# Performance work log

Hardware: AMD Instinct MI355X
Metric: run time of the kernel (lower is better)

Reference implementation:

```python
import jax, jax.numpy as jnp
import numpy as np

N = 20000      # nodes
E = 400000     # edges
D = 256        # input_dim == hidden_dim
L = 4          # num_layers
EIN = 32       # edgenet_input_dim // 2
EH = 128       # edge parser hidden
NC = 2         # num_classes
JK = L * D     # 1024
BN_EPS = 1e-5


def setup_inputs() -> dict:
    key = jax.random.key(0)
    ks = jax.random.split(key, 16)
    s = 0.05
    inp = {
        "features": jax.random.normal(ks[0], (N, D), jnp.float32),
        "edge_index": jax.random.randint(ks[1], (2, E), 0, N, dtype=jnp.int64),
        "edgenet_input": jax.random.normal(ks[2], (E, 2 * EIN), jnp.float32),
        # ChebConv weights: [layer, k, in, out] (all layers 256->256, K=3, no bias)
        "cheb_w": jax.random.normal(ks[3], (L, 3, D, D), jnp.float32) * s,
        # EdgeEncoder (PAE-style) parser: Linear(32,128)+ReLU+BN+Linear(128,128)
        "en_w1": jax.random.normal(ks[4], (EIN, EH), jnp.float32) * s,
        "en_b1": jnp.zeros((EH,), jnp.float32),
        "en_g1": jnp.ones((EH,), jnp.float32),
        "en_be1": jnp.zeros((EH,), jnp.float32),
        "en_w2": jax.random.normal(ks[5], (EH, EH), jnp.float32) * s,
        "en_b2": jnp.zeros((EH,), jnp.float32),
        # cls head: Linear(1024,256)+ReLU+BN(256)+Linear(256,2)
        "cls_w1": jax.random.normal(ks[6], (JK, 256), jnp.float32) * s,
        "cls_b1": jnp.zeros((256,), jnp.float32),
        "cls_g": jnp.ones((256,), jnp.float32),
        "cls_b": jnp.zeros((256,), jnp.float32),
        "cls_w2": jax.random.normal(ks[7], (256, NC), jnp.float32) * s,
        "cls_b2": jnp.zeros((NC,), jnp.float32),
    }
    return inp


def _bn_eval(x, g, b):
    # eval-mode BatchNorm1d with fresh running stats (mean=0, var=1)
    return x * (g / jnp.sqrt(1.0 + BN_EPS)) + b


def reference(features, edge_index, edgenet_input, cheb_w,
              en_w1, en_b1, en_g1, en_be1, en_w2, en_b2,
              cls_w1, cls_b1, cls_g, cls_b, cls_w2, cls_b2):
    row, col = edge_index[0], edge_index[1]

    # ---- EdgeEncoder (PAE): shared parser on both halves + cosine sim ----
    def parser(x):
        h = jnp.maximum(x @ en_w1 + en_b1, 0.0)
        h = _bn_eval(h, en_g1, en_be1)
        return h @ en_w2 + en_b2

    half = edgenet_input.shape[1] // 2
    h1 = parser(edgenet_input[:, :half])
    h2 = parser(edgenet_input[:, half:])
    n1 = jnp.maximum(jnp.linalg.norm(h1, axis=1), 1e-8)
    n2 = jnp.maximum(jnp.linalg.norm(h2, axis=1), 1e-8)
    cos = jnp.sum(h1 * h2, axis=1) / (n1 * n2)
    edge_weight = (cos + 1.0) * 0.5  # [E]

    # ---- ChebConv sym normalization (lambda_max=2): L_hat = -D^-1/2 A D^-1/2 ----
    deg = jax.ops.segment_sum(edge_weight, row, num_segments=N)
    dis = jnp.where(deg > 0, jax.lax.rsqrt(jnp.maximum(deg, 1e-30)), 0.0)
    norm = -dis[row] * edge_weight * dis[col]  # [E]

    def prop(x):  # out[col] += norm * x[row]
        return jax.ops.segment_sum(x[row] * norm[:, None], col, num_segments=N)

    # ---- stacked ChebConv (K=3, no bias) + ReLU + JK concat ----
    x = features
    jk = None
    for i in range(L):
        W = cheb_w[i]
        Tx0 = x
        Tx1 = prop(Tx0)
        Tx2 = 2.0 * prop(Tx1) - Tx0
        h = jnp.maximum(Tx0 @ W[0] + Tx1 @ W[1] + Tx2 @ W[2], 0.0)
        jk = h if i == 0 else jnp.concatenate([jk, h], axis=1)
        x = h

    # ---- cls head ----
    z = jnp.maximum(jk @ cls_w1 + cls_b1, 0.0)
    z = _bn_eval(z, cls_g, cls_b)
    logit = z @ cls_w2 + cls_b2
    return (logit, edge_weight)
```

## Files before the change

### kernel.cpp

```cpp
#include <hip/hip_runtime.h>

#define NN 20000
#define EE 400000
#define RSBN 0.9999950000374997f

typedef __attribute__((ext_vector_type(8))) short short8;
typedef __attribute__((ext_vector_type(8))) unsigned short ushort8;
typedef __attribute__((ext_vector_type(4))) float floatx4;

__device__ __forceinline__ short f2bf(float f) {
  union { float f; unsigned u; } v; v.f = f;
  unsigned r = v.u + 0x7fffu + ((v.u >> 16) & 1u);
  return (short)(r >> 16);
}
__device__ __forceinline__ float bf2f(unsigned short u) {
  union { unsigned u; float f; } v; v.u = ((unsigned)u) << 16;
  return v.f;
}
__device__ __forceinline__ void gl_lds16(const void* g, void* l) {
  __builtin_amdgcn_global_load_lds(
      (const __attribute__((address_space(1))) unsigned*)g,
      (__attribute__((address_space(3))) unsigned*)l, 16, 0, 0);
}

#define ASP 136
__global__ __launch_bounds__(256, 2) void edge_kernel(
    const float* __restrict__ xin, const int* __restrict__ eidx,
    const float* __restrict__ w1, const float* __restrict__ b1,
    const float* __restrict__ g1, const float* __restrict__ be1,
    const float* __restrict__ w2, const float* __restrict__ b2,
    float* __restrict__ ew_out, float* __restrict__ ew_ws,
    float* __restrict__ deg, int* __restrict__ cnt)
{
  __shared__ short w1f[8 * 64 * 8];
  __shared__ short w2f[4 * 8 * 64 * 8];
  __shared__ short as_s[128 * ASP];

  int tid = threadIdx.x;
  int lane = tid & 63;
  int wv = tid >> 6;
  int l15 = lane & 15;
  int quad = lane >> 4;

#pragma unroll
  for (int i = 0; i < 16; i++) {
    int idx = i * 256 + tid;
    int k = idx >> 7, n = idx & 127;
    int pos = ((n >> 4) * 64 + (k >> 3) * 16 + (n & 15)) * 8 + (k & 7);
    w1f[pos] = f2bf(w1[idx]);
  }
#pragma unroll
  for (int i = 0; i < 64; i++) {
    int idx = i * 256 + tid;
    int k = idx >> 7, n = idx & 127;
    int pos = (((k >> 5) * 8 + (n >> 4)) * 64 + ((k >> 3) & 3) * 16 + (n & 15)) * 8 + (k & 7);
    w2f[pos] = f2bf(w2[idx]);
  }

  float b1j[8], s1j[8], be1j[8], b2j[8];
#pragma unroll
  for (int c = 0; c < 8; c++) {
    int n = c * 16 + l15;
    b1j[c] = b1[n]; s1j[c] = g1[n] * RSBN; be1j[c] = be1[n]; b2j[c] = b2[n];
  }

  int rowbase = blockIdx.x * 128 + wv * 32;

  short8 af[2];
#pragma unroll
  for (int t = 0; t < 2; t++) {
    const float* xp = xin + (size_t)(rowbase + t * 16 + l15) * 32 + quad * 8;
    float4 v0 = *(const float4*)xp;
    float4 v1 = *(const float4*)(xp + 4);
    short8 a;
    a[0] = f2bf(v0.x); a[1] = f2bf(v0.y); a[2] = f2bf(v0.z); a[3] = f2bf(v0.w);
    a[4] = f2bf(v1.x); a[5] = f2bf(v1.y); a[6] = f2bf(v1.z); a[7] = f2bf(v1.w);
    af[t] = a;
  }

  __syncthreads();

  floatx4 acc[2][8];
#pragma unroll
  for (int t = 0; t < 2; t++)
#pragma unroll
    for (int c = 0; c < 8; c++) {
      floatx4 z = {0.f, 0.f, 0.f, 0.f};
      acc[t][c] = __builtin_amdgcn_mfma_f32_16x16x32_bf16(
          af[t], *(const short8*)&w1f[(c * 64 + lane) * 8], z, 0, 0, 0);
    }

#pragma unroll
  for (int t = 0; t < 2; t++)
#pragma unroll
    for (int c = 0; c < 8; c++)
#pragma unroll
      for (int r = 0; r < 4; r++) {
        float a = fmaxf(acc[t][c][r] + b1j[c], 0.f) * s1j[c] + be1j[c];
        as_s[(wv * 32 + t * 16 + quad * 4 + r) * ASP + c * 16 + l15] = f2bf(a);
      }

  floatx4 acc2[2][8];
#pragma unroll
  for (int t = 0; t < 2; t++)
#pragma unroll
    for (int c = 0; c < 8; c++) acc2[t][c] = (floatx4){0.f, 0.f, 0.f, 0.f};
#pragma unroll
  for (int s = 0; s < 4; s++) {
    short8 a2[2];
#pragma unroll
    for (int t = 0; t < 2; t++)
      a2[t] = *(const short8*)&as_s[(wv * 32 + t * 16 + l15) * ASP + s * 32 + quad * 8];
#pragma unroll
    for (int c = 0; c < 8; c++) {
      short8 bf = *(const short8*)&w2f[((s * 8 + c) * 64 + lane) * 8];
#pragma unroll
      for (int t = 0; t < 2; t++)
        acc2[t][c] = __builtin_amdgcn_mfma_f32_16x16x32_bf16(a2[t], bf, acc2[t][c], 0, 0, 0);
    }
  }

  float p[2][2], qq[2][2], rr[2][2];
#pragma unroll
  for (int t = 0; t < 2; t++)
#pragma unroll
    for (int i = 0; i < 2; i++) { p[t][i] = 0.f; qq[t][i] = 0.f; rr[t][i] = 0.f; }
#pragma unroll
  for (int c = 0; c < 8; c++)
#pragma unroll
    for (int t = 0; t < 2; t++)
#pragma unroll
      for (int i = 0; i < 2; i++) {
        float hx = acc2[t][c][2 * i]     + b2j[c];
        float hy = acc2[t][c][2 * i + 1] + b2j[c];
        p[t][i]  += hx * hy;
        qq[t][i] += hx * hx;
        rr[t][i] += hy * hy;
      }
#pragma unroll
  for (int m = 1; m < 16; m <<= 1)
#pragma unroll
    for (int t = 0; t < 2; t++)
#pragma unroll
      for (int i = 0; i < 2; i++) {
        p[t][i]  += __shfl_xor(p[t][i], m, 64);
        qq[t][i] += __shfl_xor(qq[t][i], m, 64);
        rr[t][i] += __shfl_xor(rr[t][i], m, 64);
      }
  if (l15 == 0) {
#pragma unroll
    for (int t = 0; t < 2; t++)
#pragma unroll
      for (int i = 0; i < 2; i++) {
        int row = rowbase + t * 16 + quad * 4 + 2 * i;
        int e = row >> 1;
        float n1 = fmaxf(sqrtf(qq[t][i]), 1e-8f);
        float n2 = fmaxf(sqrtf(rr[t][i]), 1e-8f);
        float w = (p[t][i] / (n1 * n2) + 1.f) * 0.5f;
        ew_out[e] = w;
        ew_ws[e] = w;
        atomicAdd(deg + eidx[e], w);
        atomicAdd(cnt + eidx[EE + e], 1);
      }
  }
}

__global__ __launch_bounds__(256) void fconv_kernel(const float* __restrict__ src,
                                                    unsigned short* __restrict__ dst) {
  size_t i = ((size_t)blockIdx.x * 256 + threadIdx.x) * 8;
  float4 a = *(const float4*)(src + i);
  float4 b = *(const float4*)(src + i + 4);
  ushort8 o;
  o[0] = f2bf(a.x); o[1] = f2bf(a.y); o[2] = f2bf(a.z); o[3] = f2bf(a.w);
  o[4] = f2bf(b.x); o[5] = f2bf(b.y); o[6] = f2bf(b.z); o[7] = f2bf(b.w);
  *(ushort8*)(dst + i) = o;
}

__global__ __launch_bounds__(256) void wconv_kernel(
    const float* __restrict__ cheb_w, const float* __restrict__ cls_w1,
    unsigned short* __restrict__ wtc, unsigned short* __restrict__ clsT)
{
  __shared__ unsigned short tile[64][80];
  int z = blockIdx.z;
  const float* src; unsigned short* dst; int ldk;
  if (z < 12) {
    int l = z / 3, c = z % 3;
    src = cheb_w + (size_t)z * 65536;
    dst = wtc + (size_t)l * 196608 + c * 256;
    ldk = 768;
  } else {
    int c = z - 12;
    src = cls_w1 + (size_t)c * 65536;
    dst = clsT + c * 256;
    ldk = 1024;
  }
  int t = threadIdx.x;
  int k0 = blockIdx.x * 64, n0 = blockIdx.y * 64;
#pragma unroll
  for (int pass = 0; pass < 4; pass++) {
    int kk = pass * 16 + (t >> 4);
    int nl = (t & 15) * 4;
    float4 v = *(const float4*)(src + (size_t)(k0 + kk) * 256 + n0 + nl);
    tile[nl + 0][kk] = f2bf(v.x);
    tile[nl + 1][kk] = f2bf(v.y);
    tile[nl + 2][kk] = f2bf(v.z);
    tile[nl + 3][kk] = f2bf(v.w);
  }
  __syncthreads();
  int nl = t >> 2, kc = (t & 3) * 16;
  ushort8 v0 = *(const ushort8*)&tile[nl][kc];
  ushort8 v1 = *(const ushort8*)&tile[nl][kc + 8];
  unsigned short* dp = dst + (size_t)(n0 + nl) * ldk + k0 + kc;
  *(ushort8*)dp = v0;
  *(ushort8*)(dp + 8) = v1;
}

__global__ void dis_kernel(const float* __restrict__ deg, float* __restrict__ dis) {
  int i = blockIdx.x * 256 + threadIdx.x;
  if (i < NN) {
    float d = deg[i];
    dis[i] = d > 0.f ? 1.f / sqrtf(fmaxf(d, 1e-30f)) : 0.f;
  }
}

__global__ __launch_bounds__(1024) void scan_kernel(const int* __restrict__ cnt, int* __restrict__ ptr) {
  __shared__ int sums[1024];
  int tid = threadIdx.x;
  const int n = NN;
  const int chunk = (n + 1023) / 1024;
  int base = tid * chunk;
  int s = 0;
  for (int i = 0; i < chunk; i++) { int idx = base + i; if (idx < n) s += cnt[idx]; }
  sums[tid] = s;
  __syncthreads();
  for (int off = 1; off < 1024; off <<= 1) {
    int v = (tid >= off) ? sums[tid - off] : 0;
    __syncthreads();
    sums[tid] += v;
    __syncthreads();
  }
  int run = (tid == 0) ? 0 : sums[tid - 1];
  for (int i = 0; i < chunk; i++) {
    int idx = base + i;
    if (idx < n) { ptr[idx] = run; run += cnt[idx]; }
  }
  if (tid == 1023) ptr[n] = run;
}

__global__ void fill_kernel(const int* __restrict__ eidx, const float* __restrict__ ew,
                            const float* __restrict__ dis, const int* __restrict__ ptr,
                            int* __restrict__ fill, int* __restrict__ cidx, float* __restrict__ cval) {
  int e = blockIdx.x * 256 + threadIdx.x;
  if (e < EE) {
    int r = eidx[e], c = eidx[EE + e];
    float nv = -dis[r] * ew[e] * dis[c];
    int pos = ptr[c] + atomicAdd(&fill[c], 1);
    cidx[pos] = r;
    cval[pos] = nv;
  }
}

__global__ __launch_bounds__(256) void prop_kernel(
    const unsigned short* __restrict__ x, int ldx,
    const int* __restrict__ cidx, const float* __restrict__ cval,
    const int* __restrict__ ptr,
    unsigned short* __restrict__ y, int ldy,
    float alpha, const unsigned short* __restrict__ sub, int ldsub)
{
  int c = blockIdx.x * 8 + (threadIdx.x >> 5);
  int lane5 = threadIdx.x & 31;
  int d = lane5 * 8;
  int p0 = ptr[c], p1 = ptr[c + 1];
  float a[8] = {0.f, 0.f, 0.f, 0.f, 0.f, 0.f, 0.f, 0.f};
  int p = p0;
  for (; p + 1 < p1; p += 2) {
    int r0 = cidx[p], r1 = cidx[p + 1];
    float w0 = cval[p], w1v = cval[p + 1];
    ushort8 v0 = *(const ushort8*)(x + (size_t)r0 * ldx + d);
    ushort8 v1 = *(const ushort8*)(x + (size_t)r1 * ldx + d);
#pragma unroll
    for (int j = 0; j < 8; j++) a[j] += w0 * bf2f(v0[j]) + w1v * bf2f(v1[j]);
  }
  if (p < p1) {
    int r0 = cidx[p]; float w0 = cval[p];
    ushort8 v0 = *(const ushort8*)(x + (size_t)r0 * ldx + d);
#pragma unroll
    for (int j = 0; j < 8; j++) a[j] += w0 * bf2f(v0[j]);
  }
  ushort8 o;
  if (sub) {
    ushort8 sv = *(const ushort8*)(sub + (size_t)c * ldsub + d);
#pragma unroll
    for (int j = 0; j < 8; j++) o[j] = f2bf(alpha * a[j] - bf2f(sv[j]));
  } else {
#pragma unroll
    for (int j = 0; j < 8; j++) o[j] = f2bf(a[j]);
  }
  *(ushort8*)(y + (size_t)c * ldy + d) = o;
}

__global__ __launch_bounds__(256, 2) void mgemm_kernel(
    const unsigned short* A0, const unsigned short* A1,
    const unsigned short* A2, const unsigned short* A3,
    int l0, int l1, int l2, int l3, int nchunks,
    const unsigned short* __restrict__ BT, int ldbt,
    unsigned short* __restrict__ Cb, float* __restrict__ Cf, int ldc, int M,
    const float* __restrict__ bias, const float* __restrict__ bng,
    const float* __restrict__ bnb)
{
  __shared__ short As[4 * 64 * 8];
  __shared__ short Bs[4 * 128 * 8];
  int tid = threadIdx.x;
  int lane = tid & 63;
  int wv = tid >> 6;
  int l15 = lane & 15, quad = lane >> 4;
  int wr = wv >> 1, wc = wv & 1;
  int m0 = blockIdx.x * 64, n0 = blockIdx.y * 128;

  const unsigned short* Ap[4] = {A0, A1, A2, A3};
  int Al[4] = {l0, l1, l2, l3};

  int arow = tid & 63, ac = tid >> 6;
  int brow = tid & 127, bc = tid >> 7;

  floatx4 acc[2][4];
#pragma unroll
  for (int mi = 0; mi < 2; mi++)
#pragma unroll
    for (int nj = 0; nj < 4; nj++) acc[mi][nj] = (floatx4){0.f, 0.f, 0.f, 0.f};

  for (int c = 0; c < nchunks; c++) {
    const unsigned short* Abase = Ap[c] + (size_t)(m0 + arow) * Al[c] + ac * 8;
    const unsigned short* Bbase = BT + (size_t)(n0 + brow) * ldbt + c * 256 + bc * 8;
#pragma unroll 1
    for (int kb = 0; kb < 256; kb += 32) {
      __syncthreads();
      gl_lds16(Abase + kb, &As[tid * 8]);
      gl_lds16(Bbase + kb, &Bs[tid * 8]);
      gl_lds16(Bbase + 16 + kb, &Bs[(tid + 256) * 8]);
      __syncthreads();
      short8 af[2], bfv[4];
#pragma unroll
      for (int mi = 0; mi < 2; mi++)
        af[mi] = *(const short8*)&As[(quad * 64 + wr * 32 + mi * 16 + l15) * 8];
#pragma unroll
      for (int nj = 0; nj < 4; nj++)
        bfv[nj] = *(const short8*)&Bs[(quad * 128 + wc * 64 + nj * 16 + l15) * 8];
#pragma unroll
      for (int nj = 0; nj < 4; nj++)
#pragma unroll
        for (int mi = 0; mi < 2; mi++)
          acc[mi][nj] = __builtin_amdgcn_mfma_f32_16x16x32_bf16(af[mi], bfv[nj], acc[mi][nj], 0, 0, 0);
    }
  }

  if (Cb) {
#pragma unroll
    for (int mi = 0; mi < 2; mi++)
#pragma unroll
      for (int r = 0; r < 4; r++) {
        int row = m0 + wr * 32 + mi * 16 + quad * 4 + r;
        if (row < M) {
#pragma unroll
          for (int nj = 0; nj < 4; nj++) {
            int col = n0 + wc * 64 + nj * 16 + l15;
            Cb[(size_t)row * ldc + col] = (unsigned short)f2bf(fmaxf(acc[mi][nj][r], 0.f));
          }
        }
      }
  } else {
    float bs[4], g[4], bb[4];
#pragma unroll
    for (int nj = 0; nj < 4; nj++) {
      int col = n0 + wc * 64 + nj * 16 + l15;
      bs[nj] = bias[col]; g[nj] = bng[col] * RSBN; bb[nj] = bnb[col];
    }
#pragma unroll
    for (int mi = 0; mi < 2; mi++)
#pragma unroll
      for (int r = 0; r < 4; r++) {
        int row = m0 + wr * 32 + mi * 16 + quad * 4 + r;
        if (row < M) {
#pragma unroll
          for (int nj = 0; nj < 4; nj++) {
            int col = n0 + wc * 64 + nj * 16 + l15;
            float v = fmaxf(acc[mi][nj][r] + bs[nj], 0.f) * g[nj] + bb[nj];
            Cf[(size_t)row * ldc + col] = v;
          }
        }
      }
  }
}

__global__ __launch_bounds__(256) void logit_kernel(
    const float* __restrict__ z, const float* __restrict__ w2,
    const float* __restrict__ b2, float* __restrict__ out)
{
  int node = blockIdx.x * 4 + (threadIdx.x >> 6);
  if (node >= NN) return;
  int lane = threadIdx.x & 63;
  int k = lane * 4;
  float4 zv = *(const float4*)(z + (size_t)node * 256 + k);
  float4 wa = *(const float4*)(w2 + k * 2);
  float4 wb = *(const float4*)(w2 + k * 2 + 4);
  float a0 = zv.x * wa.x + zv.y * wa.z + zv.z * wb.x + zv.w * wb.z;
  float a1 = zv.x * wa.y + zv.y * wa.w + zv.z * wb.y + zv.w * wb.w;
#pragma unroll
  for (int m = 32; m >= 1; m >>= 1) {
    a0 += __shfl_xor(a0, m, 64);
    a1 += __shfl_xor(a1, m, 64);
  }
  if (lane == 0) {
    out[(size_t)node * 2]     = a0 + b2[0];
    out[(size_t)node * 2 + 1] = a1 + b2[1];
  }
}

extern "C" void kernel_launch(void* const* d_in, const int* in_sizes, int n_in,
                              void* d_out, int out_size, void* d_ws, size_t ws_size,
                              hipStream_t stream) {
  const float* features = (const float*)d_in[0];
  const int*   eidx     = (const int*)d_in[1];
  const float* xin      = (const float*)d_in[2];
  const float* cheb_w   = (const float*)d_in[3];
  const float* en_w1    = (const float*)d_in[4];
  const float* en_b1    = (const float*)d_in[5];
  const float* en_g1    = (const float*)d_in[6];
  const float* en_be1   = (const float*)d_in[7];
  const float* en_w2    = (const float*)d_in[8];
  const float* en_b2    = (const float*)d_in[9];
  const float* cls_w1   = (const float*)d_in[10];
  const float* cls_b1   = (const float*)d_in[11];
  const float* cls_g    = (const float*)d_in[12];
  const float* cls_b    = (const float*)d_in[13];
  const float* cls_w2   = (const float*)d_in[14];
  const float* cls_b2   = (const float*)d_in[15];
  float* out = (float*)d_out;

  char* ws = (char*)d_ws;
  size_t off = 0;
  auto alloc = [&](size_t bytes) -> void* {
    void* p = ws + off;
    off += (bytes + 255) & ~(size_t)255;
    return p;
  };
  float* deg  = (float*)alloc((size_t)NN * 4);
  int*   cnt  = (int*)  alloc((size_t)NN * 4);
  int*   fil  = (int*)  alloc((size_t)NN * 4);
  size_t zero_len = off;
  float* dis  = (float*)alloc((size_t)NN * 4);
  int*   ptr  = (int*)  alloc((size_t)(NN + 1) * 4);
  float* ew   = (float*)alloc((size_t)EE * 4);
  int*   cidx = (int*)  alloc((size_t)EE * 4);
  float* cval = (float*)alloc((size_t)EE * 4);
  unsigned short* featb = (unsigned short*)alloc((size_t)NN * 256 * 2);
  unsigned short* Tx1   = (unsigned short*)alloc((size_t)NN * 256 * 2);
  unsigned short* Tx2   = (unsigned short*)alloc((size_t)NN * 256 * 2);
  unsigned short* jk    = (unsigned short*)alloc((size_t)NN * 1024 * 2);
  float* zbuf = (float*)alloc((size_t)NN * 256 * 4);
  unsigned short* wtc   = (unsigned short*)alloc((size_t)4 * 196608 * 2);
  unsigned short* clsT  = (unsigned short*)alloc((size_t)256 * 1024 * 2);
  alloc(262144);

  hipMemsetAsync(deg, 0, zero_len, stream);

  edge_kernel<<<6250, 256, 0, stream>>>(xin, eidx, en_w1, en_b1, en_g1, en_be1,
                                        en_w2, en_b2, out + (size_t)NN * 2, ew, deg, cnt);
  fconv_kernel<<<2500, 256, 0, stream>>>(features, featb);
  wconv_kernel<<<dim3(4, 4, 16), 256, 0, stream>>>(cheb_w, cls_w1, wtc, clsT);
  dis_kernel<<<(NN + 255) / 256, 256, 0, stream>>>(deg, dis);
  scan_kernel<<<1, 1024, 0, stream>>>(cnt, ptr);
  fill_kernel<<<(EE + 255) / 256, 256, 0, stream>>>(eidx, ew, dis, ptr, fil, cidx, cval);

  dim3 ggrid(313, 2);
  for (int i = 0; i < 4; i++) {
    const unsigned short* x = (i == 0) ? featb : (jk + (size_t)(i - 1) * 256);
    int ldx = (i == 0) ? 256 : 1024;
    prop_kernel<<<2500, 256, 0, stream>>>(x, ldx, cidx, cval, ptr, Tx1, 256, 1.f, nullptr, 0);
    prop_kernel<<<2500, 256, 0, stream>>>(Tx1, 256, cidx, cval, ptr, Tx2, 256, 2.f, x, ldx);
    mgemm_kernel<<<ggrid, 256, 0, stream>>>(x, Tx1, Tx2, nullptr, ldx, 256, 256, 0, 3,
                                            wtc + (size_t)i * 196608, 768,
                                            jk + (size_t)i * 256, nullptr, 1024, NN,
                                            nullptr, nullptr, nullptr);
  }

  mgemm_kernel<<<ggrid, 256, 0, stream>>>(jk, jk + 256, jk + 512, jk + 768,
                                          1024, 1024, 1024, 1024, 4, clsT, 1024,
                                          nullptr, zbuf, 256, NN,
                                          cls_b1, cls_g, cls_b);
  logit_kernel<<<NN / 4, 256, 0, stream>>>(zbuf, cls_w2, cls_b2, out);
}
```

Baseline: 745.7 us.

## Pre-convert edge MLP weights once, async-load to LDS, unroll SpMM gather

A new single-block kernel converts and swizzles the edge-encoder weights to bf16 once. Previously each of the 6250 edge_kernel blocks re-read and converted 20K floats into LDS; now each block copies the pre-swizzled buffer with global_load_lds. edge_kernel moves to 512 threads with one 16-row tile per wave, which cuts per-wave register use and raises occupancy. Separately, prop_kernel unrolls its neighbor gather by four to keep more loads in flight. The extra kernel launch and the reliance on the barrier waiting for the async LDS loads are the added risks.

New measurement: 693.4 us. 7.0% less time.

```diff
diff --git a/kernel.cpp b/kernel.cpp
--- a/kernel.cpp
+++ b/kernel.cpp
@@ -23,17 +23,37 @@
       (__attribute__((address_space(3))) unsigned*)l, 16, 0, 0);
 }
 
+__global__ __launch_bounds__(256) void ewconv_kernel(
+    const float* __restrict__ w1, const float* __restrict__ w2,
+    unsigned short* __restrict__ ewf)
+{
+  int tid = threadIdx.x;
+#pragma unroll
+  for (int i = 0; i < 16; i++) {
+    int idx = i * 256 + tid;
+    int k = idx >> 7, n = idx & 127;
+    int pos = ((n >> 4) * 64 + (k >> 3) * 16 + (n & 15)) * 8 + (k & 7);
+    ewf[pos] = f2bf(w1[idx]);
+  }
+#pragma unroll
+  for (int i = 0; i < 64; i++) {
+    int idx = i * 256 + tid;
+    int k = idx >> 7, n = idx & 127;
+    int pos = (((k >> 5) * 8 + (n >> 4)) * 64 + ((k >> 3) & 3) * 16 + (n & 15)) * 8 + (k & 7);
+    ewf[4096 + pos] = f2bf(w2[idx]);
+  }
+}
+
 #define ASP 136
-__global__ __launch_bounds__(256, 2) void edge_kernel(
+__global__ __launch_bounds__(512, 4) void edge_kernel(
     const float* __restrict__ xin, const int* __restrict__ eidx,
-    const float* __restrict__ w1, const float* __restrict__ b1,
-    const float* __restrict__ g1, const float* __restrict__ be1,
-    const float* __restrict__ w2, const float* __restrict__ b2,
+    const unsigned short* __restrict__ ewf,
+    const float* __restrict__ b1, const float* __restrict__ g1,
+    const float* __restrict__ be1, const float* __restrict__ b2,
     float* __restrict__ ew_out, float* __restrict__ ew_ws,
     float* __restrict__ deg, int* __restrict__ cnt)
 {
-  __shared__ short w1f[8 * 64 * 8];
-  __shared__ short w2f[4 * 8 * 64 * 8];
+  __shared__ short wbuf[20480];
   __shared__ short as_s[128 * ASP];
 
   int tid = threadIdx.x;
@@ -43,19 +63,11 @@
   int quad = lane >> 4;
 
 #pragma unroll
-  for (int i = 0; i < 16; i++) {
-    int idx = i * 256 + tid;
-    int k = idx >> 7, n = idx & 127;
-    int pos = ((n >> 4) * 64 + (k >> 3) * 16 + (n & 15)) * 8 + (k & 7);
-    w1f[pos] = f2bf(w1[idx]);
-  }
-#pragma unroll
-  for (int i = 0; i < 64; i++) {
-    int idx = i * 256 + tid;
-    int k = idx >> 7, n = idx & 127;
-    int pos = (((k >> 5) * 8 + (n >> 4)) * 64 + ((k >> 3) & 3) * 16 + (n & 15)) * 8 + (k & 7);
-    w2f[pos] = f2bf(w2[idx]);
-  }
+  for (int i = 0; i < 5; i++)
+    gl_lds16(ewf + (i * 512 + tid) * 8, &wbuf[(i * 512 + tid) * 8]);
+
+  const short* w1f = wbuf;
+  const short* w2f = wbuf + 4096;
 
   float b1j[8], s1j[8], be1j[8], b2j[8];
 #pragma unroll
@@ -64,104 +76,82 @@
     b1j[c] = b1[n]; s1j[c] = g1[n] * RSBN; be1j[c] = be1[n]; b2j[c] = b2[n];
   }
 
-  int rowbase = blockIdx.x * 128 + wv * 32;
-
-  short8 af[2];
-#pragma unroll
-  for (int t = 0; t < 2; t++) {
-    const float* xp = xin + (size_t)(rowbase + t * 16 + l15) * 32 + quad * 8;
+  int rowbase = blockIdx.x * 128 + wv * 16;
+
+  short8 af;
+  {
+    const float* xp = xin + (size_t)(rowbase + l15) * 32 + quad * 8;
     float4 v0 = *(const float4*)xp;
     float4 v1 = *(const float4*)(xp + 4);
-    short8 a;
-    a[0] = f2bf(v0.x); a[1] = f2bf(v0.y); a[2] = f2bf(v0.z); a[3] = f2bf(v0.w);
-    a[4] = f2bf(v1.x); a[5] = f2bf(v1.y); a[6] = f2bf(v1.z); a[7] = f2bf(v1.w);
-    af[t] = a;
+    af[0] = f2bf(v0.x); af[1] = f2bf(v0.y); af[2] = f2bf(v0.z); af[3] = f2bf(v0.w);
+    af[4] = f2bf(v1.x); af[5] = f2bf(v1.y); af[6] = f2bf(v1.z); af[7] = f2bf(v1.w);
   }
 
   __syncthreads();
 
-  floatx4 acc[2][8];
-#pragma unroll
-  for (int t = 0; t < 2; t++)
-#pragma unroll
-    for (int c = 0; c < 8; c++) {
-      floatx4 z = {0.f, 0.f, 0.f, 0.f};
-      acc[t][c] = __builtin_amdgcn_mfma_f32_16x16x32_bf16(
-          af[t], *(const short8*)&w1f[(c * 64 + lane) * 8], z, 0, 0, 0);
-    }
-
-#pragma unroll
-  for (int t = 0; t < 2; t++)
-#pragma unroll
-    for (int c = 0; c < 8; c++)
-#pragma unroll
-      for (int r = 0; r < 4; r++) {
-        float a = fmaxf(acc[t][c][r] + b1j[c], 0.f) * s1j[c] + be1j[c];
-        as_s[(wv * 32 + t * 16 + quad * 4 + r) * ASP + c * 16 + l15] = f2bf(a);
-      }
-
-  floatx4 acc2[2][8];
-#pragma unroll
-  for (int t = 0; t < 2; t++)
-#pragma unroll
-    for (int c = 0; c < 8; c++) acc2[t][c] = (floatx4){0.f, 0.f, 0.f, 0.f};
+  floatx4 acc[8];
+#pragma unroll
+  for (int c = 0; c < 8; c++) {
+    floatx4 z = {0.f, 0.f, 0.f, 0.f};
+    acc[c] = __builtin_amdgcn_mfma_f32_16x16x32_bf16(
+        af, *(const short8*)&w1f[(c * 64 + lane) * 8], z, 0, 0, 0);
+  }
+
+#pragma unroll
+  for (int c = 0; c < 8; c++)
+#pragma unroll
+    for (int r = 0; r < 4; r++) {
+      float a = fmaxf(acc[c][r] + b1j[c], 0.f) * s1j[c] + be1j[c];
+      as_s[(wv * 16 + quad * 4 + r) * ASP + c * 16 + l15] = f2bf(a);
+    }
+
+  floatx4 acc2[8];
+#pragma unroll
+  for (int c = 0; c < 8; c++) acc2[c] = (floatx4){0.f, 0.f, 0.f, 0.f};
 #pragma unroll
   for (int s = 0; s < 4; s++) {
-    short8 a2[2];
-#pragma unroll
-    for (int t = 0; t < 2; t++)
-      a2[t] = *(const short8*)&as_s[(wv * 32 + t * 16 + l15) * ASP + s * 32 + quad * 8];
+    short8 a2 = *(const short8*)&as_s[(wv * 16 + l15) * ASP + s * 32 + quad * 8];
 #pragma unroll
     for (int c = 0; c < 8; c++) {
       short8 bf = *(const short8*)&w2f[((s * 8 + c) * 64 + lane) * 8];
-#pragma unroll
-      for (int t = 0; t < 2; t++)
-        acc2[t][c] = __builtin_amdgcn_mfma_f32_16x16x32_bf16(a2[t], bf, acc2[t][c], 0, 0, 0);
-    }
-  }
-
-  float p[2][2], qq[2][2], rr[2][2];
-#pragma unroll
-  for (int t = 0; t < 2; t++)
-#pragma unroll
-    for (int i = 0; i < 2; i++) { p[t][i] = 0.f; qq[t][i] = 0.f; rr[t][i] = 0.f; }
+      acc2[c] = __builtin_amdgcn_mfma_f32_16x16x32_bf16(a2, bf, acc2[c], 0, 0, 0);
+    }
+  }
+
+  float p[2], qq[2], rr[2];
+#pragma unroll
+  for (int i = 0; i < 2; i++) { p[i] = 0.f; qq[i] = 0.f; rr[i] = 0.f; }
 #pragma unroll
   for (int c = 0; c < 8; c++)
 #pragma unroll
-    for (int t = 0; t < 2; t++)
-#pragma unroll
-      for (int i = 0; i < 2; i++) {
-        float hx = acc2[t][c][2 * i]     + b2j[c];
-        float hy = acc2[t][c][2 * i + 1] + b2j[c];
-        p[t][i]  += hx * hy;
-        qq[t][i] += hx * hx;
-        rr[t][i] += hy * hy;
-      }
+    for (int i = 0; i < 2; i++) {
+      float hx = acc2[c][2 * i]     + b2j[c];
+      float hy = acc2[c][2 * i + 1] + b2j[c];
+      p[i]  += hx * hy;
+      qq[i] += hx * hx;
+      rr[i] += hy * hy;
+    }
 #pragma unroll
   for (int m = 1; m < 16; m <<= 1)
 #pragma unroll
-    for (int t = 0; t < 2; t++)
-#pragma unroll
-      for (int i = 0; i < 2; i++) {
-        p[t][i]  += __shfl_xor(p[t][i], m, 64);
-        qq[t][i] += __shfl_xor(qq[t][i], m, 64);
-        rr[t][i] += __shfl_xor(rr[t][i], m, 64);
-      }
+    for (int i = 0; i < 2; i++) {
+      p[i]  += __shfl_xor(p[i], m, 64);
+      qq[i] += __shfl_xor(qq[i], m, 64);
+      rr[i] += __shfl_xor(rr[i], m, 64);
+    }
   if (l15 == 0) {
 #pragma unroll
-    for (int t = 0; t < 2; t++)
-#pragma unroll
-      for (int i = 0; i < 2; i++) {
-        int row = rowbase + t * 16 + quad * 4 + 2 * i;
-        int e = row >> 1;
-        float n1 = fmaxf(sqrtf(qq[t][i]), 1e-8f);
-        float n2 = fmaxf(sqrtf(rr[t][i]), 1e-8f);
-        float w = (p[t][i] / (n1 * n2) + 1.f) * 0.5f;
-        ew_out[e] = w;
-        ew_ws[e] = w;
-        atomicAdd(deg + eidx[e], w);
-        atomicAdd(cnt + eidx[EE + e], 1);
-      }
+    for (int i = 0; i < 2; i++) {
+      int row = rowbase + quad * 4 + 2 * i;
+      int e = row >> 1;
+      float n1 = fmaxf(sqrtf(qq[i]), 1e-8f);
+      float n2 = fmaxf(sqrtf(rr[i]), 1e-8f);
+      float w = (p[i] / (n1 * n2) + 1.f) * 0.5f;
+      ew_out[e] = w;
+      ew_ws[e] = w;
+      atomicAdd(deg + eidx[e], w);
+      atomicAdd(cnt + eidx[EE + e], 1);
+    }
   }
 }
 
@@ -273,15 +263,18 @@
   int p0 = ptr[c], p1 = ptr[c + 1];
   float a[8] = {0.f, 0.f, 0.f, 0.f, 0.f, 0.f, 0.f, 0.f};
   int p = p0;
-  for (; p + 1 < p1; p += 2) {
-    int r0 = cidx[p], r1 = cidx[p + 1];
-    float w0 = cval[p], w1v = cval[p + 1];
+  for (; p + 3 < p1; p += 4) {
+    int r0 = cidx[p], r1 = cidx[p + 1], r2 = cidx[p + 2], r3 = cidx[p + 3];
+    float w0 = cval[p], w1v = cval[p + 1], w2v = cval[p + 2], w3v = cval[p + 3];
     ushort8 v0 = *(const ushort8*)(x + (size_t)r0 * ldx + d);
     ushort8 v1 = *(const ushort8*)(x + (size_t)r1 * ldx + d);
-#pragma unroll
-    for (int j = 0; j < 8; j++) a[j] += w0 * bf2f(v0[j]) + w1v * bf2f(v1[j]);
-  }
-  if (p < p1) {
+    ushort8 v2 = *(const ushort8*)(x + (size_t)r2 * ldx + d);
+    ushort8 v3 = *(const ushort8*)(x + (size_t)r3 * ldx + d);
+#pragma unroll
+    for (int j = 0; j < 8; j++)
+      a[j] += w0 * bf2f(v0[j]) + w1v * bf2f(v1[j]) + w2v * bf2f(v2[j]) + w3v * bf2f(v3[j]);
+  }
+  for (; p < p1; p++) {
     int r0 = cidx[p]; float w0 = cval[p];
     ushort8 v0 = *(const ushort8*)(x + (size_t)r0 * ldx + d);
 #pragma unroll
@@ -460,12 +453,14 @@
   float* zbuf = (float*)alloc((size_t)NN * 256 * 4);
   unsigned short* wtc   = (unsigned short*)alloc((size_t)4 * 196608 * 2);
   unsigned short* clsT  = (unsigned short*)alloc((size_t)256 * 1024 * 2);
+  unsigned short* ewf   = (unsigned short*)alloc((size_t)20480 * 2);
   alloc(262144);
 
   hipMemsetAsync(deg, 0, zero_len, stream);
 
-  edge_kernel<<<6250, 256, 0, stream>>>(xin, eidx, en_w1, en_b1, en_g1, en_be1,
-                                        en_w2, en_b2, out + (size_t)NN * 2, ew, deg, cnt);
+  ewconv_kernel<<<1, 256, 0, stream>>>(en_w1, en_w2, ewf);
+  edge_kernel<<<6250, 512, 0, stream>>>(xin, eidx, ewf, en_b1, en_g1, en_be1, en_b2,
+                                        out + (size_t)NN * 2, ew, deg, cnt);
   fconv_kernel<<<2500, 256, 0, stream>>>(features, featb);
   wconv_kernel<<<dim3(4, 4, 16), 256, 0, stream>>>(cheb_w, cls_w1, wtc, clsT);
   dis_kernel<<<(NN + 255) / 256, 256, 0, stream>>>(deg, dis);
```
